# Kernel tuning notes

Measured on AMD Instinct MI355X. Metric: run time of the kernel, lower is better.

## Reference

```python
import jax, jax.numpy as jnp
import numpy as np

N_HEADS = 8
D_EMBED = 512
D_HEAD = D_EMBED // N_HEADS


def setup_inputs() -> dict:
    key = jax.random.key(0)
    ks = jax.random.split(key, 5)
    B, S, D = 8, 2048, D_EMBED
    scale_in = 1.0 / np.sqrt(D)
    x = jax.random.normal(ks[0], (B, S, D), dtype=jnp.float32)
    # torch nn.Linear weights: (out_features, in_features)
    w_in = jax.random.normal(ks[1], (3 * D, D), dtype=jnp.float32) * scale_in
    b_in = jax.random.normal(ks[2], (3 * D,), dtype=jnp.float32) * scale_in
    w_out = jax.random.normal(ks[3], (D, D), dtype=jnp.float32) * scale_in
    b_out = jax.random.normal(ks[4], (D,), dtype=jnp.float32) * scale_in
    return {"x": x, "w_in": w_in, "b_in": b_in, "w_out": w_out, "b_out": b_out}


def reference(x, w_in, b_in, w_out, b_out):
    B, S, D = x.shape
    H, Dh = N_HEADS, D_HEAD
    # fused QKV projection (torch Linear: x @ W^T + b)
    qkv = x @ w_in.T + b_in                     # (B, S, 3D)
    q, k, v = jnp.split(qkv, 3, axis=-1)        # each (B, S, D)
    # split heads -> (B, H, S, Dh)
    def heads(t):
        return t.reshape(B, S, H, Dh).transpose(0, 2, 1, 3)
    q, k, v = heads(q), heads(k), heads(v)
    # scaled dot-product attention (full matrix, as in source)
    scores = jnp.einsum("bhqd,bhkd->bhqk", q, k) / jnp.sqrt(jnp.float32(Dh))
    weights = jax.nn.softmax(scores, axis=-1)   # (B, H, S, S)
    out = jnp.einsum("bhqk,bhkd->bhqd", weights, v)
    out = out.transpose(0, 2, 1, 3).reshape(B, S, D)
    return out @ w_out.T + b_out
```

## Files before the change

kernel.cpp:

```cpp
#include <hip/hip_runtime.h>
#include <stdint.h>

#define SEQ   2048
#define DEMB  512
#define NH    8
#define DH    64
#define BATCH 8
#define M_ROWS (BATCH * SEQ)
#define QKLD  1024
#define QSCALE 0.18033688011112042f

typedef __attribute__((ext_vector_type(8))) __bf16 bf16x8;
typedef __attribute__((ext_vector_type(4))) __bf16 bf16x4;
typedef __attribute__((ext_vector_type(4))) float  f32x4;
typedef __attribute__((ext_vector_type(8))) uint16_t u16x8;

__device__ __forceinline__ void gll16(const __bf16* g, __bf16* l) {
    __builtin_amdgcn_global_load_lds(
        (__attribute__((address_space(1))) void*)(__bf16*)g,
        (__attribute__((address_space(3))) void*)l, 16, 0, 0);
}

__device__ __forceinline__ bf16x8 ld8(const __bf16* p) {
    return *(const bf16x8*)p;
}

__device__ __forceinline__ uint32_t pkbf(float a, float b) {
    uint32_t ua = __builtin_bit_cast(uint32_t, a) + 0x8000u;
    uint32_t ub = __builtin_bit_cast(uint32_t, b) + 0x8000u;
    return __builtin_amdgcn_perm(ub, ua, 0x07060302);
}

__device__ __forceinline__ int sw(int row, int chunk) {
    return row * 64 + ((chunk ^ (row & 7)) << 3);
}

__device__ __forceinline__ void stage_gll_sw(const __bf16* g, int gld,
                                             __bf16* l, int wave, int lane) {
    const int lr = lane >> 3;
    const int scol = ((lane & 7) ^ lr) * 8;
    #pragma unroll
    for (int i = 0; i < 2; i++) {
        const int r0 = i * 32 + wave * 8;
        gll16(g + (size_t)(r0 + lr) * gld + scol, l + r0 * 64);
    }
}

__device__ __forceinline__ void stage_gll(const __bf16* src, __bf16* dst,
                                          int ld, int wave, int lane) {
    const int srow = lane >> 3, scol = (lane & 7) * 8;
    #pragma unroll
    for (int i = 0; i < 4; i++) {
        const int r0 = (i * 4 + wave) * 8;
        gll16(src + (size_t)(r0 + srow) * ld + scol, dst + r0 * 64);
    }
}

#define NXQ (M_ROWS * DEMB / 4)
#define NWQ (3 * DEMB * DEMB / 4)
#define NOQ (DEMB * DEMB / 4)

__global__ __launch_bounds__(256)
void cvt_all(const float* __restrict__ x, const float* __restrict__ w_in,
             __bf16* __restrict__ xb, __bf16* __restrict__ wb) {
    const int i = blockIdx.x * 256 + threadIdx.x;
    const float4* src;
    bf16x4* dst;
    if (i < NXQ) { src = (const float4*)x + i;         dst = (bf16x4*)xb + i; }
    else if (i < NXQ + NWQ) {
        const int j = i - NXQ;
        src = (const float4*)w_in + j;  dst = (bf16x4*)wb + j;
    } else return;
    const float4 v = *src;
    bf16x4 b;
    b[0] = (__bf16)v.x; b[1] = (__bf16)v.y;
    b[2] = (__bf16)v.z; b[3] = (__bf16)v.w;
    *dst = b;
}

__global__ __launch_bounds__(256)
void cvt_wout(const float* __restrict__ w, __bf16* __restrict__ wb) {
    const int i = blockIdx.x * 256 + threadIdx.x;
    if (i < NOQ) {
        const float4 v = ((const float4*)w)[i];
        bf16x4 b;
        b[0] = (__bf16)v.x; b[1] = (__bf16)v.y;
        b[2] = (__bf16)v.z; b[3] = (__bf16)v.w;
        ((bf16x4*)wb)[i] = b;
    }
}

__global__ __launch_bounds__(256)
void gemm_qkv(const __bf16* __restrict__ A, const __bf16* __restrict__ W,
              const float* __restrict__ bias, __bf16* __restrict__ qk,
              __bf16* __restrict__ vt) {
    constexpr int K = DEMB;
    __shared__ __align__(16) __bf16 SM[128 * 128];
    __bf16* As = SM;
    __bf16* Bs = SM + 128 * 64;

    const int tid  = threadIdx.x;
    const int wave = tid >> 6, lane = tid & 63;
    const int quad = lane >> 4, l16 = lane & 15;
    const int m0 = blockIdx.x * 128, n0 = blockIdx.y * 128;
    const int wm = wave & 1, wn = wave >> 1;

    f32x4 acc[4][4] = {};

    for (int k0 = 0; k0 < K; k0 += 64) {
        __syncthreads();
        stage_gll(A + (size_t)m0 * K + k0, As, K, wave, lane);
        stage_gll(W + (size_t)n0 * K + k0, Bs, K, wave, lane);
        __syncthreads();
        #pragma unroll
        for (int ks = 0; ks < 2; ks++) {
            bf16x8 af[4], bf[4];
            #pragma unroll
            for (int t = 0; t < 4; t++) {
                af[t] = ld8(&As[(wm * 64 + t * 16 + l16) * 64 + ks * 32 + quad * 8]);
                bf[t] = ld8(&Bs[(wn * 64 + t * 16 + l16) * 64 + ks * 32 + quad * 8]);
            }
            #pragma unroll
            for (int i = 0; i < 4; i++)
                #pragma unroll
                for (int j = 0; j < 4; j++)
                    acc[i][j] = __builtin_amdgcn_mfma_f32_16x16x32_bf16(
                        af[i], bf[j], acc[i][j], 0, 0, 0);
        }
    }

    if (n0 < QKLD) {
        const float scl = (n0 < DEMB) ? QSCALE : 1.0f;
        #pragma unroll
        for (int j = 0; j < 4; j++) {
            const int n = n0 + wn * 64 + j * 16 + l16;
            const float bv = bias[n];
            #pragma unroll
            for (int i = 0; i < 4; i++) {
                const int mr = m0 + wm * 64 + i * 16 + quad * 4;
                #pragma unroll
                for (int r = 0; r < 4; r++)
                    qk[(size_t)(mr + r) * QKLD + n] = (__bf16)((acc[i][j][r] + bv) * scl);
            }
        }
    } else {
        __syncthreads();
        const int hd0 = n0 - QKLD;
        const int bb = m0 >> 11, s0 = m0 & (SEQ - 1);
        #pragma unroll
        for (int j = 0; j < 4; j++) {
            const int n = n0 + wn * 64 + j * 16 + l16;
            const float bv = bias[n];
            const int hdl = wn * 64 + j * 16 + l16;
            #pragma unroll
            for (int i = 0; i < 4; i++) {
                const int sl = wm * 64 + i * 16 + quad * 4;
                bf16x4 pk;
                #pragma unroll
                for (int r = 0; r < 4; r++)
                    pk[r] = (__bf16)(acc[i][j][r] + bv);
                const int chunk = sl >> 3;
                const int phys = (((chunk & 7) ^ (hdl & 7)) | (chunk & 8));
                *(bf16x4*)(&SM[hdl * 128 + phys * 8 + (sl & 7)]) = pk;
            }
        }
        __syncthreads();
        const int g = tid >> 4, li = tid & 15;
        #pragma unroll
        for (int it = 0; it < 8; it++) {
            const int row = it * 16 + g;
            const int phys = (((li & 7) ^ (row & 7)) | (li & 8));
            bf16x8 v = ld8(&SM[row * 128 + phys * 8]);
            *(bf16x8*)(vt + ((size_t)(bb * DEMB + hd0 + row)) * SEQ + s0 + li * 8) = v;
        }
    }
}

__global__ __launch_bounds__(256)
void attn_flash(const __bf16* __restrict__ qk, const __bf16* __restrict__ vt,
                __bf16* __restrict__ outp) {
    const int qt = blockIdx.x, h = blockIdx.y, b = blockIdx.z;
    const int tid  = threadIdx.x;
    const int wave = tid >> 6, lane = tid & 63;
    const int quad = lane >> 4, l16 = lane & 15;

    __shared__ __align__(16) __bf16 Ks[2][64 * 64];
    __shared__ __align__(16) __bf16 Vt[2][64 * 64];
    __shared__ __align__(16) __bf16 Ps[4][16 * 64];

    const size_t brow = (size_t)b * SEQ;
    const int q0 = qt * 128 + wave * 32;
    const __bf16* kbase = qk + brow * QKLD + DEMB + h * DH;
    const __bf16* vbase = vt + ((size_t)(b * DEMB + h * DH)) * SEQ;

    const u16x8 one16 = {0x3F80, 0x3F80, 0x3F80, 0x3F80,
                         0x3F80, 0x3F80, 0x3F80, 0x3F80};
    const bf16x8 ONES = __builtin_bit_cast(bf16x8, one16);

    bf16x8 qf[2][2];
    #pragma unroll
    for (int qb = 0; qb < 2; qb++) {
        const __bf16* qp = qk + (brow + q0 + qb * 16 + l16) * QKLD + h * DH + quad * 8;
        qf[qb][0] = ld8(qp);
        qf[qb][1] = ld8(qp + 32);
    }

    f32x4 o[2][4] = {};
    f32x4 osum[2] = {};

    stage_gll_sw(kbase, QKLD, Ks[0], wave, lane);
    stage_gll_sw(vbase, SEQ,  Vt[0], wave, lane);

    for (int t = 0; t < SEQ / 64; t++) {
        __syncthreads();
        if (t + 1 < SEQ / 64) {
            const int nb = (t + 1) & 1;
            stage_gll_sw(kbase + (size_t)(t + 1) * 64 * QKLD, QKLD, Ks[nb], wave, lane);
            stage_gll_sw(vbase + (t + 1) * 64,                SEQ,  Vt[nb], wave, lane);
        }
        const int buf = t & 1;

        f32x4 st[2][4];
        #pragma unroll
        for (int kt = 0; kt < 4; kt++) {
            bf16x8 kf0 = ld8(&Ks[buf][sw(kt * 16 + l16, quad)]);
            bf16x8 kf1 = ld8(&Ks[buf][sw(kt * 16 + l16, 4 + quad)]);
            #pragma unroll
            for (int qb = 0; qb < 2; qb++) {
                f32x4 c = {};
                c = __builtin_amdgcn_mfma_f32_16x16x32_bf16(kf0, qf[qb][0], c, 0, 0, 0);
                c = __builtin_amdgcn_mfma_f32_16x16x32_bf16(kf1, qf[qb][1], c, 0, 0, 0);
                st[qb][kt] = c;
            }
        }

        bf16x8 pf[2][2];
        #pragma unroll
        for (int qb = 0; qb < 2; qb++) {
            #pragma unroll
            for (int kt = 0; kt < 4; kt++) {
                const float p0 = __builtin_amdgcn_exp2f(st[qb][kt][0]);
                const float p1 = __builtin_amdgcn_exp2f(st[qb][kt][1]);
                const float p2 = __builtin_amdgcn_exp2f(st[qb][kt][2]);
                const float p3 = __builtin_amdgcn_exp2f(st[qb][kt][3]);
                uint2 w;
                w.x = pkbf(p0, p1);
                w.y = pkbf(p2, p3);
                const int chunk = kt * 2 + (quad >> 1);
                *(uint2*)(&Ps[wave][l16 * 64 + ((chunk ^ (l16 & 7)) << 3) + (quad & 1) * 4]) = w;
            }
            pf[qb][0] = ld8(&Ps[wave][sw(l16, quad)]);
            pf[qb][1] = ld8(&Ps[wave][sw(l16, 4 + quad)]);
            osum[qb] = __builtin_amdgcn_mfma_f32_16x16x32_bf16(pf[qb][0], ONES, osum[qb], 0, 0, 0);
            osum[qb] = __builtin_amdgcn_mfma_f32_16x16x32_bf16(pf[qb][1], ONES, osum[qb], 0, 0, 0);
        }

        #pragma unroll
        for (int db = 0; db < 4; db++) {
            bf16x8 vf0 = ld8(&Vt[buf][sw(db * 16 + l16, quad)]);
            bf16x8 vf1 = ld8(&Vt[buf][sw(db * 16 + l16, 4 + quad)]);
            #pragma unroll
            for (int qb = 0; qb < 2; qb++) {
                o[qb][db] = __builtin_amdgcn_mfma_f32_16x16x32_bf16(pf[qb][0], vf0, o[qb][db], 0, 0, 0);
                o[qb][db] = __builtin_amdgcn_mfma_f32_16x16x32_bf16(pf[qb][1], vf1, o[qb][db], 0, 0, 0);
            }
        }
    }

    #pragma unroll
    for (int qb = 0; qb < 2; qb++)
        #pragma unroll
        for (int r = 0; r < 4; r++) {
            const float linv = __builtin_amdgcn_rcpf(osum[qb][r]);
            const int q = q0 + qb * 16 + quad * 4 + r;
            #pragma unroll
            for (int db = 0; db < 4; db++)
                outp[(brow + q) * DEMB + h * DH + db * 16 + l16] =
                    (__bf16)(o[qb][db][r] * linv);
        }
}

__global__ __launch_bounds__(256)
void gemm_out(const __bf16* __restrict__ A, const __bf16* __restrict__ W,
              const float* __restrict__ bias, float* __restrict__ C,
              int N, int K) {
    __shared__ __align__(16) __bf16 As[128 * 64];
    __shared__ __align__(16) __bf16 Bs[128 * 64];

    const int tid  = threadIdx.x;
    const int wave = tid >> 6, lane = tid & 63;
    const int quad = lane >> 4, l16 = lane & 15;
    const int m0 = blockIdx.x * 128, n0 = blockIdx.y * 128;
    const int wm = wave & 1, wn = wave >> 1;

    f32x4 acc[4][4] = {};

    for (int k0 = 0; k0 < K; k0 += 64) {
        __syncthreads();
        stage_gll(A + (size_t)m0 * K + k0, As, K, wave, lane);
        stage_gll(W + (size_t)n0 * K + k0, Bs, K, wave, lane);
        __syncthreads();
        #pragma unroll
        for (int ks = 0; ks < 2; ks++) {
            bf16x8 af[4], bf[4];
            #pragma unroll
            for (int t = 0; t < 4; t++) {
                af[t] = ld8(&As[(wm * 64 + t * 16 + l16) * 64 + ks * 32 + quad * 8]);
                bf[t] = ld8(&Bs[(wn * 64 + t * 16 + l16) * 64 + ks * 32 + quad * 8]);
            }
            #pragma unroll
            for (int i = 0; i < 4; i++)
                #pragma unroll
                for (int j = 0; j < 4; j++)
                    acc[i][j] = __builtin_amdgcn_mfma_f32_16x16x32_bf16(
                        af[i], bf[j], acc[i][j], 0, 0, 0);
        }
    }

    #pragma unroll
    for (int j = 0; j < 4; j++) {
        const int n = n0 + wn * 64 + j * 16 + l16;
        const float bv = bias[n];
        #pragma unroll
        for (int i = 0; i < 4; i++) {
            const int mr = m0 + wm * 64 + i * 16 + quad * 4;
            #pragma unroll
            for (int r = 0; r < 4; r++)
                C[(size_t)(mr + r) * N + n] = acc[i][j][r] + bv;
        }
    }
}

extern "C" void kernel_launch(void* const* d_in, const int* in_sizes, int n_in,
                              void* d_out, int out_size, void* d_ws, size_t ws_size,
                              hipStream_t stream) {
    const float* x     = (const float*)d_in[0];
    const float* w_in  = (const float*)d_in[1];
    const float* b_in  = (const float*)d_in[2];
    const float* w_out = (const float*)d_in[3];
    const float* b_out = (const float*)d_in[4];

    __bf16* qk   = (__bf16*)d_ws;
    __bf16* vtb  = qk + (size_t)M_ROWS * QKLD;
    __bf16* xbuf = vtb + (size_t)BATCH * DEMB * SEQ;
    __bf16* aout = xbuf;
    __bf16* woutb = vtb;
    __bf16* winb = (__bf16*)((char*)d_out + 24u * 1024 * 1024);
    float*  outp = (float*)d_out;

    cvt_all<<<(NXQ + NWQ + 255) / 256, 256, 0, stream>>>(x, w_in, xbuf, winb);
    gemm_qkv<<<dim3(M_ROWS / 128, 12), 256, 0, stream>>>(xbuf, winb, b_in, qk, vtb);
    attn_flash<<<dim3(SEQ / 128, NH, BATCH), 256, 0, stream>>>(qk, vtb, aout);
    cvt_wout<<<NOQ / 256, 256, 0, stream>>>(w_out, woutb);
    gemm_out<<<dim3(M_ROWS / 128, DEMB / 128), 256, 0, stream>>>(
        aout, woutb, b_out, outp, DEMB, DEMB);
}
```

Baseline: 256.7 us.

## Replace LDS round-trip for P with cross-lane permlane swaps and hw bf16 pack

Measured after the change: 252.1 us. Within noise of the previous version (-1.8%).

```diff
diff --git a/kernel.cpp b/kernel.cpp
--- a/kernel.cpp
+++ b/kernel.cpp
@@ -14,6 +14,7 @@
 typedef __attribute__((ext_vector_type(4))) __bf16 bf16x4;
 typedef __attribute__((ext_vector_type(4))) float  f32x4;
 typedef __attribute__((ext_vector_type(8))) uint16_t u16x8;
+typedef __attribute__((ext_vector_type(4))) uint32_t u32x4;
 
 __device__ __forceinline__ void gll16(const __bf16* g, __bf16* l) {
     __builtin_amdgcn_global_load_lds(
@@ -25,10 +26,10 @@
     return *(const bf16x8*)p;
 }
 
-__device__ __forceinline__ uint32_t pkbf(float a, float b) {
-    uint32_t ua = __builtin_bit_cast(uint32_t, a) + 0x8000u;
-    uint32_t ub = __builtin_bit_cast(uint32_t, b) + 0x8000u;
-    return __builtin_amdgcn_perm(ub, ua, 0x07060302);
+__device__ __forceinline__ uint32_t cvtpk(float lo, float hi) {
+    uint32_t r;
+    asm("v_cvt_pk_bf16_f32 %0, %1, %2" : "=v"(r) : "v"(lo), "v"(hi));
+    return r;
 }
 
 __device__ __forceinline__ int sw(int row, int chunk) {
@@ -186,7 +187,6 @@
 
     __shared__ __align__(16) __bf16 Ks[2][64 * 64];
     __shared__ __align__(16) __bf16 Vt[2][64 * 64];
-    __shared__ __align__(16) __bf16 Ps[4][16 * 64];
 
     const size_t brow = (size_t)b * SEQ;
     const int q0 = qt * 128 + wave * 32;
@@ -221,6 +221,7 @@
         const int buf = t & 1;
 
         f32x4 st[2][4];
+        __builtin_amdgcn_s_setprio(1);
         #pragma unroll
         for (int kt = 0; kt < 4; kt++) {
             bf16x8 kf0 = ld8(&Ks[buf][sw(kt * 16 + l16, quad)]);
@@ -233,28 +234,38 @@
                 st[qb][kt] = c;
             }
         }
+        __builtin_amdgcn_s_setprio(0);
 
         bf16x8 pf[2][2];
         #pragma unroll
         for (int qb = 0; qb < 2; qb++) {
+            uint32_t pk[4][2];
             #pragma unroll
             for (int kt = 0; kt < 4; kt++) {
                 const float p0 = __builtin_amdgcn_exp2f(st[qb][kt][0]);
                 const float p1 = __builtin_amdgcn_exp2f(st[qb][kt][1]);
                 const float p2 = __builtin_amdgcn_exp2f(st[qb][kt][2]);
                 const float p3 = __builtin_amdgcn_exp2f(st[qb][kt][3]);
-                uint2 w;
-                w.x = pkbf(p0, p1);
-                w.y = pkbf(p2, p3);
-                const int chunk = kt * 2 + (quad >> 1);
-                *(uint2*)(&Ps[wave][l16 * 64 + ((chunk ^ (l16 & 7)) << 3) + (quad & 1) * 4]) = w;
-            }
-            pf[qb][0] = ld8(&Ps[wave][sw(l16, quad)]);
-            pf[qb][1] = ld8(&Ps[wave][sw(l16, 4 + quad)]);
+                pk[kt][0] = cvtpk(p0, p1);
+                pk[kt][1] = cvtpk(p2, p3);
+            }
+            #pragma unroll
+            for (int f = 0; f < 2; f++) {
+                uint32_t a0 = pk[2 * f][0], b0 = pk[2 * f + 1][0];
+                asm("v_permlane32_swap_b32 %0, %1" : "+v"(a0), "+v"(b0));
+                asm("v_permlane16_swap_b32 %0, %1" : "+v"(a0), "+v"(b0));
+                uint32_t a1 = pk[2 * f][1], b1 = pk[2 * f + 1][1];
+                asm("v_permlane32_swap_b32 %0, %1" : "+v"(a1), "+v"(b1));
+                asm("v_permlane16_swap_b32 %0, %1" : "+v"(a1), "+v"(b1));
+                u32x4 d;
+                d[0] = a0; d[1] = a1; d[2] = b0; d[3] = b1;
+                pf[qb][f] = __builtin_bit_cast(bf16x8, d);
+            }
             osum[qb] = __builtin_amdgcn_mfma_f32_16x16x32_bf16(pf[qb][0], ONES, osum[qb], 0, 0, 0);
             osum[qb] = __builtin_amdgcn_mfma_f32_16x16x32_bf16(pf[qb][1], ONES, osum[qb], 0, 0, 0);
         }
 
+        __builtin_amdgcn_s_setprio(1);
         #pragma unroll
         for (int db = 0; db < 4; db++) {
             bf16x8 vf0 = ld8(&Vt[buf][sw(db * 16 + l16, quad)]);
@@ -265,6 +276,7 @@
                 o[qb][db] = __builtin_amdgcn_mfma_f32_16x16x32_bf16(pf[qb][1], vf1, o[qb][db], 0, 0, 0);
             }
         }
+        __builtin_amdgcn_s_setprio(0);
     }
 
     #pragma unroll
```
